# Kernel optimization log

Measured on AMD Instinct MI355X. Metric: run time of the kernel, lower is better.

Reference implementation:

```python
import jax, jax.numpy as jnp
import numpy as np

L_SEQ = 512
BATCH = 16
D_IN = 41
H = 800
ALPHABET_SIZE = 20
# standard RGN backbone geometry (picometers / radians): N-CA, CA-C, C-N
BOND_LENGTHS = np.array([145.801, 152.326, 132.868], dtype=np.float32)
BOND_ANGLES = np.array([2.124, 1.941, 2.028], dtype=np.float32)


def _lstm_dir(x, W_ih, W_hh, b_ih, b_hh, reverse):
    # x: [L, B, D]; PyTorch gate order i, f, g, o
    B = x.shape[1]
    Hh = W_hh.shape[1]
    xs = x[::-1] if reverse else x
    pre = jnp.einsum('lbd,gd->lbg', xs, W_ih) + b_ih + b_hh  # [L, B, 4H]

    def step(carry, p):
        h, c = carry
        g = p + h @ W_hh.T
        i, f, gg, o = jnp.split(g, 4, axis=-1)
        c = jax.nn.sigmoid(f) * c + jax.nn.sigmoid(i) * jnp.tanh(gg)
        h = jax.nn.sigmoid(o) * jnp.tanh(c)
        return (h, c), h

    h0 = jnp.zeros((B, Hh), x.dtype)
    _, hs = jax.lax.scan(step, (h0, h0), pre)
    return hs[::-1] if reverse else hs


def _normalize(v):
    return v / (jnp.linalg.norm(v, axis=-1, keepdims=True) + 1e-8)


def calculate_dihedrals(p, alphabet):
    # p: [L, B, A] mixture weights; alphabet: [A, 3] learned dihedral angles
    return jnp.arctan2(p @ jnp.sin(alphabet), p @ jnp.cos(alphabet))  # [L, B, 3]


def calculate_coordinates(dihedrals):
    # dihedrals: [L, B, 3] -> backbone coords [3L, B, 3] via sequential NeRF extension
    L, B, _ = dihedrals.shape
    phi = jnp.transpose(dihedrals, (0, 2, 1)).reshape(L * 3, B)  # [3L, B]
    r = jnp.asarray(np.tile(BOND_LENGTHS, L))       # [3L]
    theta = jnp.asarray(np.tile(BOND_ANGLES, L))    # [3L]
    # initial reference frame (three seed atoms)
    a = jnp.zeros((B, 3), dihedrals.dtype)
    b = jnp.tile(jnp.array([BOND_LENGTHS[0], 0.0, 0.0], dihedrals.dtype), (B, 1))
    ang = np.pi - BOND_ANGLES[0]
    c = b + jnp.array([BOND_LENGTHS[1] * np.cos(ang), BOND_LENGTHS[1] * np.sin(ang), 0.0], dihedrals.dtype)

    def step(carry, inp):
        p_a, p_b, p_c = carry
        r_i, th_i, ph_i = inp  # scalar, scalar, [B]
        st, ct = jnp.sin(th_i), jnp.cos(th_i)
        d2 = jnp.stack([-r_i * ct * jnp.ones_like(ph_i),
                        r_i * st * jnp.cos(ph_i),
                        r_i * st * jnp.sin(ph_i)], axis=-1)      # [B, 3]
        bc = _normalize(p_c - p_b)
        n = _normalize(jnp.cross(p_b - p_a, bc))
        m = jnp.stack([bc, jnp.cross(n, bc), n], axis=-1)        # [B, 3, 3]
        d = jnp.einsum('bij,bj->bi', m, d2) + p_c
        return (p_b, p_c, d), d

    _, coords = jax.lax.scan(step, (a, b, c), (r, theta, phi))
    return coords  # [3L, B, 3]


def setup_inputs() -> dict:
    keys = iter(jax.random.split(jax.random.key(0), 24))
    s = 1.0 / np.sqrt(H)

    def u(shape):
        return jax.random.uniform(next(keys), shape, jnp.float32, -s, s)

    inp = {'x': jax.random.normal(next(keys), (BATCH, L_SEQ, D_IN), jnp.float32)}
    for layer, din in ((0, D_IN), (1, 2 * H)):
        for d in ('f', 'b'):
            inp['W_ih_l%d%s' % (layer, d)] = u((4 * H, din))
            inp['W_hh_l%d%s' % (layer, d)] = u((4 * H, H))
            inp['b_ih_l%d%s' % (layer, d)] = u((4 * H,))
            inp['b_hh_l%d%s' % (layer, d)] = u((4 * H,))
    inp['W_lin'] = u((ALPHABET_SIZE, 2 * H))
    inp['b_lin'] = u((ALPHABET_SIZE,))
    inp['alphabet'] = jax.random.uniform(next(keys), (ALPHABET_SIZE, 3), jnp.float32, -np.pi, np.pi)
    return inp


def reference(x, W_ih_l0f, W_hh_l0f, b_ih_l0f, b_hh_l0f,
              W_ih_l0b, W_hh_l0b, b_ih_l0b, b_hh_l0b,
              W_ih_l1f, W_hh_l1f, b_ih_l1f, b_hh_l1f,
              W_ih_l1b, W_hh_l1b, b_ih_l1b, b_hh_l1b,
              W_lin, b_lin, alphabet):
    xs = jnp.transpose(x, (1, 0, 2))  # [L, B, D] (seq-major like nn.LSTM default)
    hf = _lstm_dir(xs, W_ih_l0f, W_hh_l0f, b_ih_l0f, b_hh_l0f, False)
    hb = _lstm_dir(xs, W_ih_l0b, W_hh_l0b, b_ih_l0b, b_hh_l0b, True)
    h1 = jnp.concatenate([hf, hb], axis=-1)  # [L, B, 2H] (dropout=0.4 off in eval)
    hf2 = _lstm_dir(h1, W_ih_l1f, W_hh_l1f, b_ih_l1f, b_hh_l1f, False)
    hb2 = _lstm_dir(h1, W_ih_l1b, W_hh_l1b, b_ih_l1b, b_hh_l1b, True)
    out = jnp.concatenate([hf2, hb2], axis=-1)  # [L, B, 2H]
    logits = out @ W_lin.T + b_lin              # [L, B, ALPHABET_SIZE]
    p = jax.nn.softmax(logits, axis=1)          # faithful: nn.Softmax(dim=1)
    dih = calculate_dihedrals(p, alphabet)      # [L, B, 3]
    return calculate_coordinates(dih)           # [3L, B, 3]
```

## Files before the change

### kernel.cpp

```cpp
#include <hip/hip_runtime.h>
#include <math.h>

#define L_SEQ 512
#define BATCH 16
#define D_IN  41
#define HD    800
#define G4    3200
#define A2H   1600
#define NA    20
#define NWG   50

#define OFF_A   ((size_t)0)
#define OFF_B   (OFF_A + (size_t)L_SEQ * BATCH * G4)
#define OFF_H   (OFF_B + (size_t)L_SEQ * BATCH * G4)
#define OFF_DIH (OFF_H + (size_t)L_SEQ * BATCH * A2H)
#define OFF_BAR (OFF_DIH + (size_t)L_SEQ * BATCH * 3)
#define FLG_STRIDE 32
#define NREP 8
#define DIR_STRIDE (NREP * NWG * FLG_STRIDE)
#define LAUNCH_STRIDE (2 * DIR_STRIDE)

static __device__ __forceinline__ float sigf(float x) {
    return 1.0f / (1.0f + __expf(-x));
}

static __device__ __forceinline__ void fbar3(int* flg, int wg, int v) {
    __syncthreads();
    if (threadIdx.x < NREP)
        __hip_atomic_store(flg + ((int)threadIdx.x * NWG + wg) * FLG_STRIDE, v,
                           __ATOMIC_RELAXED, __HIP_MEMORY_SCOPE_AGENT);
    if (threadIdx.x < 64) {
        int* base = flg + ((wg & (NREP - 1)) * NWG) * FLG_STRIDE;
        for (;;) {
            int v1 = (threadIdx.x < NWG)
                         ? __hip_atomic_load(base + (int)threadIdx.x * FLG_STRIDE,
                                             __ATOMIC_RELAXED, __HIP_MEMORY_SCOPE_AGENT)
                         : v;
            if (__all(v1 >= v)) break;
        }
    }
    __syncthreads();
}

__global__ void init_bar_kernel(int* bar) {
    for (int i = blockIdx.x * 256 + threadIdx.x; i < 2 * LAUNCH_STRIDE;
         i += gridDim.x * 256)
        bar[i] = 0;
}

__global__ void pre0_kernel(const float* __restrict__ x,
                            const float* __restrict__ Wf, const float* __restrict__ bif,
                            const float* __restrict__ bhf,
                            const float* __restrict__ Wb, const float* __restrict__ bib,
                            const float* __restrict__ bhb,
                            float* __restrict__ outF, float* __restrict__ outB) {
    const int tid = threadIdx.x;
    const int wg = blockIdx.x * 4 + (tid >> 6);
    if (wg >= NWG) return;
    const int rl = tid & 63;
    const int gate = rl >> 4, j = rl & 15;
    const int g = gate * 800 + wg * 16 + j;
    const int m = blockIdx.y;
    const int dir = blockIdx.z;
    const int b = m & 15, t = m >> 4;
    const float* W  = dir ? Wb  : Wf;
    const float* bi = dir ? bib : bif;
    const float* bh = dir ? bhb : bhf;
    float acc = bi[g] + bh[g];
    const float* xr = x + ((size_t)b * L_SEQ + t) * D_IN;
    const float* wr = W + (size_t)g * D_IN;
    #pragma unroll
    for (int d = 0; d < D_IN; ++d) acc = fmaf(xr[d], wr[d], acc);
    (dir ? outB : outF)[((size_t)wg * (L_SEQ * BATCH) + m) * 64 + rl] = acc;
}

__launch_bounds__(512, 1)
__global__ void recur_kernel(const float* __restrict__ preF, const float* __restrict__ preB,
                             const float* __restrict__ WhhF, const float* __restrict__ WhhB,
                             float* __restrict__ hout, int* __restrict__ bar) {
    __shared__ float uni[17920];
    __shared__ float gates[1024];
    const int tid = threadIdx.x;
    const int dir = blockIdx.x & 1;
    const int wg  = blockIdx.x >> 1;
    const int j0  = wg * 16;
    const float* pre = dir ? preB : preF;
    const float* Whh = dir ? WhhB : WhhF;
    int* flg = bar + dir * DIR_STRIDE;

    const int q = tid >> 5, c = tid & 31;
    float w[4][25];
    #pragma unroll
    for (int gi = 0; gi < 4; ++gi) {
        const float* wr = Whh + (size_t)(gi * HD + j0 + q) * HD + c;
        #pragma unroll
        for (int kk = 0; kk < 25; ++kk) w[gi][kk] = wr[kk * 32];
    }
    float cstate = 0.0f;

    const int b2 = tid >> 5, r2w2 = tid & 31;
    const int q2 = r2w2 >> 1, u2 = r2w2 & 1;

    const float* pre_wg = pre + (size_t)wg * (L_SEQ * BATCH) * 64;

    int ofs[7], lds[7];
    #pragma unroll
    for (int i = 0; i < 6; ++i) {
        int g = tid * 4 + i * 2048;
        int b = g / 800;
        int k = g - 800 * b;
        ofs[i] = 4 * (b * A2H + k);
        lds[i] = k * 17 + b;
    }
    {
        int g = 12288 + tid;
        int b = g / 800;
        int k = g - 800 * b;
        ofs[6] = 4 * (b * A2H + k);
        lds[6] = k * 17 + b;
    }

    for (int it = 0; it < L_SEQ; ++it) {
        const int t = dir ? (L_SEQ - 1 - it) : it;

        if (it == 0) {
            for (int i = tid; i < 13600; i += 512) uni[i] = 0.0f;
        } else {
            const int tprev = dir ? (L_SEQ - it) : (it - 1);
            const float* hsrc = hout + ((size_t)tprev * BATCH) * A2H + dir * HD;
            float4 rr[6];
            float r1f;
            asm volatile(
                "global_load_dwordx4 %0, %7, %14 sc0 sc1\n\t"
                "global_load_dwordx4 %1, %8, %14 sc0 sc1\n\t"
                "global_load_dwordx4 %2, %9, %14 sc0 sc1\n\t"
                "global_load_dwordx4 %3, %10, %14 sc0 sc1\n\t"
                "global_load_dwordx4 %4, %11, %14 sc0 sc1\n\t"
                "global_load_dwordx4 %5, %12, %14 sc0 sc1\n\t"
                "global_load_dword %6, %13, %14 sc0 sc1\n\t"
                "s_waitcnt vmcnt(0)"
                : "=&v"(rr[0]), "=&v"(rr[1]), "=&v"(rr[2]), "=&v"(rr[3]),
                  "=&v"(rr[4]), "=&v"(rr[5]), "=&v"(r1f)
                : "v"(ofs[0]), "v"(ofs[1]), "v"(ofs[2]), "v"(ofs[3]),
                  "v"(ofs[4]), "v"(ofs[5]), "v"(ofs[6]), "s"(hsrc)
                : "memory");
            #pragma unroll
            for (int i = 0; i < 6; ++i) {
                uni[lds[i]]      = rr[i].x;
                uni[lds[i] + 17] = rr[i].y;
                uni[lds[i] + 34] = rr[i].z;
                uni[lds[i] + 51] = rr[i].w;
            }
            uni[lds[6]] = r1f;
        }

        float pv[2];
        #pragma unroll
        for (int half = 0; half < 2; ++half) {
            const int rl_o = (2 * half + u2) * 16 + q2;
            pv[half] = pre_wg[((size_t)t * BATCH + b2) * 64 + rl_o];
        }
        __syncthreads();

        float acc[4][16];
        #pragma unroll
        for (int gi = 0; gi < 4; ++gi)
            #pragma unroll
            for (int b = 0; b < 16; ++b) acc[gi][b] = 0.0f;
        #pragma unroll
        for (int kk = 0; kk < 25; ++kk) {
            const int kb = (c + kk * 32) * 17;
            float hreg[16];
            #pragma unroll
            for (int b = 0; b < 16; ++b) hreg[b] = uni[kb + b];
            #pragma unroll
            for (int gi = 0; gi < 4; ++gi)
                #pragma unroll
                for (int b = 0; b < 16; ++b)
                    acc[gi][b] = fmaf(w[gi][kk], hreg[b], acc[gi][b]);
        }
        __syncthreads();

        #pragma unroll
        for (int half = 0; half < 2; ++half) {
            #pragma unroll
            for (int u = 0; u < 2; ++u) {
                const int r2w = q * 2 + u;
                #pragma unroll
                for (int b = 0; b < 16; ++b)
                    uni[(b * 32 + r2w) * 35 + c] = acc[2 * half + u][b];
            }
            __syncthreads();
            {
                float s = pv[half];
                const int base = (b2 * 32 + r2w2) * 35;
                #pragma unroll
                for (int cc = 0; cc < 32; ++cc) s += uni[base + cc];
                const int rl_o = (2 * half + u2) * 16 + q2;
                gates[rl_o * 16 + b2] = s;
            }
            __syncthreads();
        }

        if (tid < 256) {
            const int jj = tid >> 4, b = tid & 15;
            float ig = gates[(0 * 16 + jj) * 16 + b];
            float fg = gates[(1 * 16 + jj) * 16 + b];
            float gg = gates[(2 * 16 + jj) * 16 + b];
            float og = gates[(3 * 16 + jj) * 16 + b];
            float cn = sigf(fg) * cstate + sigf(ig) * tanhf(gg);
            cstate = cn;
            float hn = sigf(og) * tanhf(cn);
            __hip_atomic_store(&hout[((size_t)t * BATCH + b) * A2H + dir * HD + j0 + jj],
                               hn, __ATOMIC_RELAXED, __HIP_MEMORY_SCOPE_AGENT);
        }
        if (it < L_SEQ - 1) fbar3(flg, wg, it + 1);
    }
}

static __device__ __forceinline__ int permn(int np) {
    return ((np & 63) >> 4) * 800 + (np >> 6) * 16 + (np & 15);
}

__launch_bounds__(256)
__global__ void gemm_pre1_kernel(const float* __restrict__ Ah,
                                 const float* __restrict__ WF, const float* __restrict__ biF,
                                 const float* __restrict__ bhF,
                                 const float* __restrict__ WB, const float* __restrict__ biB,
                                 const float* __restrict__ bhB,
                                 float* __restrict__ CF, float* __restrict__ CB) {
    __shared__ float As[16][132];
    __shared__ float Bs[16][132];
    const int dir = blockIdx.z;
    const float* Bw = dir ? WB : WF;
    const float* bi = dir ? biB : biF;
    const float* bh = dir ? bhB : bhF;
    float* C = dir ? CB : CF;
    const int n0 = blockIdx.x * 128;
    const int m0 = blockIdx.y * 128;
    const int tid = threadIdx.x;
    const int mt = tid >> 4, nt = tid & 15;
    const int r = tid >> 2, kq = tid & 3;
    const size_t nr0 = (size_t)permn(n0 + r) * A2H;
    const size_t nr1 = (size_t)permn(n0 + r + 64) * A2H;

    float acc[8][8];
    #pragma unroll
    for (int i = 0; i < 8; ++i)
        #pragma unroll
        for (int j = 0; j < 8; ++j) acc[i][j] = 0.0f;

    for (int k0 = 0; k0 < A2H; k0 += 16) {
        float4 a0 = *(const float4*)(Ah + (size_t)(m0 + r) * A2H + k0 + kq * 4);
        float4 a1 = *(const float4*)(Ah + (size_t)(m0 + r + 64) * A2H + k0 + kq * 4);
        float4 b0 = *(const float4*)(Bw + nr0 + k0 + kq * 4);
        float4 b1 = *(const float4*)(Bw + nr1 + k0 + kq * 4);
        __syncthreads();
        As[kq * 4 + 0][r] = a0.x;  As[kq * 4 + 1][r] = a0.y;
        As[kq * 4 + 2][r] = a0.z;  As[kq * 4 + 3][r] = a0.w;
        As[kq * 4 + 0][r + 64] = a1.x;  As[kq * 4 + 1][r + 64] = a1.y;
        As[kq * 4 + 2][r + 64] = a1.z;  As[kq * 4 + 3][r + 64] = a1.w;
        Bs[kq * 4 + 0][r] = b0.x;  Bs[kq * 4 + 1][r] = b0.y;
        Bs[kq * 4 + 2][r] = b0.z;  Bs[kq * 4 + 3][r] = b0.w;
        Bs[kq * 4 + 0][r + 64] = b1.x;  Bs[kq * 4 + 1][r + 64] = b1.y;
        Bs[kq * 4 + 2][r + 64] = b1.z;  Bs[kq * 4 + 3][r + 64] = b1.w;
        __syncthreads();
        #pragma unroll
        for (int kk = 0; kk < 16; ++kk) {
            float av[8], bv[8];
            #pragma unroll
            for (int j = 0; j < 8; ++j) av[j] = As[kk][mt * 8 + j];
            #pragma unroll
            for (int j = 0; j < 8; ++j) bv[j] = Bs[kk][nt * 8 + j];
            #pragma unroll
            for (int i = 0; i < 8; ++i)
                #pragma unroll
                for (int j = 0; j < 8; ++j)
                    acc[i][j] = fmaf(av[i], bv[j], acc[i][j]);
        }
    }
    float bias[8];
    #pragma unroll
    for (int j = 0; j < 8; ++j) {
        int n = permn(n0 + nt * 8 + j);
        bias[j] = bi[n] + bh[n];
    }
    const int npb = n0 + nt * 8;
    const int seg = npb >> 6;
    const int lo  = npb & 63;
    #pragma unroll
    for (int i = 0; i < 8; ++i) {
        float* dst = C + ((size_t)seg * (L_SEQ * BATCH) + (m0 + mt * 8 + i)) * 64 + lo;
        #pragma unroll
        for (int j = 0; j < 8; ++j) dst[j] = acc[i][j] + bias[j];
    }
}

__global__ void head_kernel(const float* __restrict__ out2,
                            const float* __restrict__ Wlin,
                            const float* __restrict__ blin,
                            const float* __restrict__ alphabet,
                            float* __restrict__ dih) {
    __shared__ float lg[16][21];
    __shared__ float sal[20][3], cal[20][3];
    const int t = blockIdx.x;
    const int tid = threadIdx.x;
    if (tid < 60) {
        int a = tid / 3, d = tid - 3 * (tid / 3);
        float v = alphabet[a * 3 + d];
        sal[a][d] = sinf(v);
        cal[a][d] = cosf(v);
    }
    const int b = tid / 20, a = tid - 20 * (tid / 20);
    const float* orow = out2 + ((size_t)t * BATCH + b) * A2H;
    const float* wrow = Wlin + (size_t)a * A2H;
    float s = blin[a];
    for (int k = 0; k < A2H; k += 4) {
        float4 ov = *(const float4*)(orow + k);
        float4 wv = *(const float4*)(wrow + k);
        s = fmaf(ov.x, wv.x, s);
        s = fmaf(ov.y, wv.y, s);
        s = fmaf(ov.z, wv.z, s);
        s = fmaf(ov.w, wv.w, s);
    }
    lg[b][a] = s;
    __syncthreads();
    if (tid < NA) {
        float mx = -1e30f;
        #pragma unroll
        for (int bb = 0; bb < BATCH; ++bb) mx = fmaxf(mx, lg[bb][tid]);
        float sum = 0.0f;
        #pragma unroll
        for (int bb = 0; bb < BATCH; ++bb) {
            float e = expf(lg[bb][tid] - mx);
            lg[bb][tid] = e;
            sum += e;
        }
        float inv = 1.0f / sum;
        #pragma unroll
        for (int bb = 0; bb < BATCH; ++bb) lg[bb][tid] *= inv;
    }
    __syncthreads();
    if (tid < 48) {
        int bb = tid / 3, dd = tid - 3 * (tid / 3);
        float ss = 0.0f, cc = 0.0f;
        #pragma unroll
        for (int aa = 0; aa < NA; ++aa) {
            float p = lg[bb][aa];
            ss = fmaf(p, sal[aa][dd], ss);
            cc = fmaf(p, cal[aa][dd], cc);
        }
        dih[((size_t)t * BATCH + bb) * 3 + dd] = atan2f(ss, cc);
    }
}

__global__ void nerf_kernel(const float* __restrict__ dih, float* __restrict__ out) {
    const int b = threadIdx.x;
    if (b >= BATCH) return;
    const float BL0 = 145.801f, BL1 = 152.326f, BL2 = 132.868f;
    const float BA0 = 2.124f,   BA1 = 1.941f,   BA2 = 2.028f;
    const float rr[3] = {BL0, BL1, BL2};
    const float st3[3] = {sinf(BA0), sinf(BA1), sinf(BA2)};
    const float ct3[3] = {cosf(BA0), cosf(BA1), cosf(BA2)};
    float ax = 0.f, ay = 0.f, az = 0.f;
    float bx = BL0, by = 0.f, bz = 0.f;
    float ang = 3.14159265358979323846f - BA0;
    float cx = bx + BL1 * cosf(ang), cy = BL1 * sinf(ang), cz = 0.f;
    for (int l = 0; l < L_SEQ; ++l) {
        #pragma unroll
        for (int d = 0; d < 3; ++d) {
            const int s = l * 3 + d;
            const float r = rr[d], st = st3[d], ct = ct3[d];
            float ph = dih[((size_t)l * BATCH + b) * 3 + d];
            float sp, cp;
            __sincosf(ph, &sp, &cp);
            float d2x = -r * ct, d2y = r * st * cp, d2z = r * st * sp;
            float bcx = cx - bx, bcy = cy - by, bcz = cz - bz;
            float inv = 1.0f / (sqrtf(bcx * bcx + bcy * bcy + bcz * bcz) + 1e-8f);
            bcx *= inv; bcy *= inv; bcz *= inv;
            float abx = bx - ax, aby = by - ay, abz = bz - az;
            float nx = aby * bcz - abz * bcy;
            float ny = abz * bcx - abx * bcz;
            float nz = abx * bcy - aby * bcx;
            inv = 1.0f / (sqrtf(nx * nx + ny * ny + nz * nz) + 1e-8f);
            nx *= inv; ny *= inv; nz *= inv;
            float m1x = ny * bcz - nz * bcy;
            float m1y = nz * bcx - nx * bcz;
            float m1z = nx * bcy - ny * bcx;
            float dx = bcx * d2x + m1x * d2y + nx * d2z + cx;
            float dy = bcy * d2x + m1y * d2y + ny * d2z + cy;
            float dz = bcz * d2x + m1z * d2y + nz * d2z + cz;
            size_t o = ((size_t)s * BATCH + b) * 3;
            out[o + 0] = dx; out[o + 1] = dy; out[o + 2] = dz;
            ax = bx; ay = by; az = bz;
            bx = cx; by = cy; bz = cz;
            cx = dx; cy = dy; cz = dz;
        }
    }
}

extern "C" void kernel_launch(void* const* d_in, const int* in_sizes, int n_in,
                              void* d_out, int out_size, void* d_ws, size_t ws_size,
                              hipStream_t stream) {
    (void)in_sizes; (void)n_in; (void)out_size; (void)ws_size;
    const float* x        = (const float*)d_in[0];
    const float* W_ih_l0f = (const float*)d_in[1];
    const float* W_hh_l0f = (const float*)d_in[2];
    const float* b_ih_l0f = (const float*)d_in[3];
    const float* b_hh_l0f = (const float*)d_in[4];
    const float* W_ih_l0b = (const float*)d_in[5];
    const float* W_hh_l0b = (const float*)d_in[6];
    const float* b_ih_l0b = (const float*)d_in[7];
    const float* b_hh_l0b = (const float*)d_in[8];
    const float* W_ih_l1f = (const float*)d_in[9];
    const float* W_hh_l1f = (const float*)d_in[10];
    const float* b_ih_l1f = (const float*)d_in[11];
    const float* b_hh_l1f = (const float*)d_in[12];
    const float* W_ih_l1b = (const float*)d_in[13];
    const float* W_hh_l1b = (const float*)d_in[14];
    const float* b_ih_l1b = (const float*)d_in[15];
    const float* b_hh_l1b = (const float*)d_in[16];
    const float* W_lin    = (const float*)d_in[17];
    const float* b_lin    = (const float*)d_in[18];
    const float* alphabet = (const float*)d_in[19];

    float* ws  = (float*)d_ws;
    float* bufA = ws + OFF_A;
    float* bufB = ws + OFF_B;
    float* h12  = ws + OFF_H;
    float* dih  = ws + OFF_DIH;
    int*   bar  = (int*)(ws + OFF_BAR);

    hipLaunchKernelGGL(init_bar_kernel, dim3(32), dim3(256), 0, stream, bar);

    hipLaunchKernelGGL(pre0_kernel, dim3(13, L_SEQ * BATCH, 2), dim3(256), 0, stream,
                       x, W_ih_l0f, b_ih_l0f, b_hh_l0f,
                       W_ih_l0b, b_ih_l0b, b_hh_l0b, bufA, bufB);

    {
        const float* a0 = bufA; const float* a1 = bufB;
        const float* a2 = W_hh_l0f; const float* a3 = W_hh_l0b;
        float* a4 = h12; int* a5 = bar;
        void* args[] = {&a0, &a1, &a2, &a3, &a4, &a5};
        hipError_t e = hipLaunchCooperativeKernel((const void*)recur_kernel, dim3(100),
                                                  dim3(512), args, 0, stream);
        (void)e;
    }

    hipLaunchKernelGGL(gemm_pre1_kernel, dim3(G4 / 128, (L_SEQ * BATCH) / 128, 2),
                       dim3(256), 0, stream,
                       h12, W_ih_l1f, b_ih_l1f, b_hh_l1f,
                       W_ih_l1b, b_ih_l1b, b_hh_l1b, bufA, bufB);

    {
        const float* a0 = bufA; const float* a1 = bufB;
        const float* a2 = W_hh_l1f; const float* a3 = W_hh_l1b;
        float* a4 = h12; int* a5 = bar + LAUNCH_STRIDE;
        void* args[] = {&a0, &a1, &a2, &a3, &a4, &a5};
        hipError_t e = hipLaunchCooperativeKernel((const void*)recur_kernel, dim3(100),
                                                  dim3(512), args, 0, stream);
        (void)e;
    }

    hipLaunchKernelGGL(head_kernel, dim3(L_SEQ), dim3(320), 0, stream,
                       h12, W_lin, b_lin, alphabet, dih);

    hipLaunchKernelGGL(nerf_kernel, dim3(1), dim3(64), 0, stream,
                       dih, (float*)d_out);
}
```

Measured before the change: 15.66 ms.

## Restructure recurrent kernel k-split for float4 LDS reads and single-pass reduction

Remaps threads in the persistent LSTM recurrence so each lane owns a contiguous 25-element k-slice, with h stored in LDS at stride 20 so four float4 loads fetch all 16 batch values. The cross-lane partial-sum reduction now goes through one shared buffer in a single pass instead of two halves with extra barriers, and the gate nonlinearity reads sums straight from registers. This cuts LDS instruction count and the number of barriers per timestep, at the cost of doubling the LDS footprint and possible bank conflicts in the new layout.

```diff
diff --git a/kernel.cpp b/kernel.cpp
--- a/kernel.cpp
+++ b/kernel.cpp
@@ -78,8 +78,7 @@
 __global__ void recur_kernel(const float* __restrict__ preF, const float* __restrict__ preB,
                              const float* __restrict__ WhhF, const float* __restrict__ WhhB,
                              float* __restrict__ hout, int* __restrict__ bar) {
-    __shared__ float uni[17920];
-    __shared__ float gates[1024];
+    __shared__ float uni[35840];
     const int tid = threadIdx.x;
     const int dir = blockIdx.x & 1;
     const int wg  = blockIdx.x >> 1;
@@ -88,18 +87,22 @@
     const float* Whh = dir ? WhhB : WhhF;
     int* flg = bar + dir * DIR_STRIDE;
 
-    const int q = tid >> 5, c = tid & 31;
+    const int wv = tid >> 6;
+    const int lane = tid & 63;
+    const int q = lane >> 2;
+    const int c = lane & 3;
+    const int k0 = wv * 100 + c * 25;
+    const int col2 = (4 * wv + c + 4 * q) & 31;
+
     float w[4][25];
     #pragma unroll
     for (int gi = 0; gi < 4; ++gi) {
-        const float* wr = Whh + (size_t)(gi * HD + j0 + q) * HD + c;
-        #pragma unroll
-        for (int kk = 0; kk < 25; ++kk) w[gi][kk] = wr[kk * 32];
+        const float* wr = Whh + (size_t)(gi * HD + j0 + q) * HD + k0;
+        #pragma unroll
+        for (int kk = 0; kk < 25; ++kk) w[gi][kk] = wr[kk];
     }
     float cstate = 0.0f;
-
-    const int b2 = tid >> 5, r2w2 = tid & 31;
-    const int q2 = r2w2 >> 1, u2 = r2w2 & 1;
+    const int jj2 = (tid >> 4) & 15, b2 = tid & 15;
 
     const float* pre_wg = pre + (size_t)wg * (L_SEQ * BATCH) * 64;
 
@@ -110,21 +113,21 @@
         int b = g / 800;
         int k = g - 800 * b;
         ofs[i] = 4 * (b * A2H + k);
-        lds[i] = k * 17 + b;
+        lds[i] = k * 20 + b;
     }
     {
         int g = 12288 + tid;
         int b = g / 800;
         int k = g - 800 * b;
         ofs[6] = 4 * (b * A2H + k);
-        lds[6] = k * 17 + b;
+        lds[6] = k * 20 + b;
     }
 
     for (int it = 0; it < L_SEQ; ++it) {
         const int t = dir ? (L_SEQ - 1 - it) : it;
 
         if (it == 0) {
-            for (int i = tid; i < 13600; i += 512) uni[i] = 0.0f;
+            for (int i = tid; i < 16000; i += 512) uni[i] = 0.0f;
         } else {
             const int tprev = dir ? (L_SEQ - it) : (it - 1);
             const float* hsrc = hout + ((size_t)tprev * BATCH) * A2H + dir * HD;
@@ -147,18 +150,18 @@
             #pragma unroll
             for (int i = 0; i < 6; ++i) {
                 uni[lds[i]]      = rr[i].x;
-                uni[lds[i] + 17] = rr[i].y;
-                uni[lds[i] + 34] = rr[i].z;
-                uni[lds[i] + 51] = rr[i].w;
+                uni[lds[i] + 20] = rr[i].y;
+                uni[lds[i] + 40] = rr[i].z;
+                uni[lds[i] + 60] = rr[i].w;
             }
             uni[lds[6]] = r1f;
         }
 
-        float pv[2];
-        #pragma unroll
-        for (int half = 0; half < 2; ++half) {
-            const int rl_o = (2 * half + u2) * 16 + q2;
-            pv[half] = pre_wg[((size_t)t * BATCH + b2) * 64 + rl_o];
+        float pv[4];
+        if (tid < 256) {
+            #pragma unroll
+            for (int gi = 0; gi < 4; ++gi)
+                pv[gi] = pre_wg[((size_t)t * BATCH + b2) * 64 + gi * 16 + jj2];
         }
         __syncthreads();
 
@@ -169,10 +172,13 @@
             for (int b = 0; b < 16; ++b) acc[gi][b] = 0.0f;
         #pragma unroll
         for (int kk = 0; kk < 25; ++kk) {
-            const int kb = (c + kk * 32) * 17;
-            float hreg[16];
-            #pragma unroll
-            for (int b = 0; b < 16; ++b) hreg[b] = uni[kb + b];
+            const float* hp = &uni[(k0 + kk) * 20];
+            float4 h0 = *(const float4*)(hp);
+            float4 h1 = *(const float4*)(hp + 4);
+            float4 h2 = *(const float4*)(hp + 8);
+            float4 h3 = *(const float4*)(hp + 12);
+            float hreg[16] = {h0.x, h0.y, h0.z, h0.w, h1.x, h1.y, h1.z, h1.w,
+                              h2.x, h2.y, h2.z, h2.w, h3.x, h3.y, h3.z, h3.w};
             #pragma unroll
             for (int gi = 0; gi < 4; ++gi)
                 #pragma unroll
@@ -182,36 +188,26 @@
         __syncthreads();
 
         #pragma unroll
-        for (int half = 0; half < 2; ++half) {
-            #pragma unroll
-            for (int u = 0; u < 2; ++u) {
-                const int r2w = q * 2 + u;
+        for (int gi = 0; gi < 4; ++gi)
+            #pragma unroll
+            for (int b = 0; b < 16; ++b)
+                uni[((gi * 16 + q) * 16 + b) * 35 + col2] = acc[gi][b];
+        __syncthreads();
+
+        if (tid < 256) {
+            float s[4];
+            #pragma unroll
+            for (int gi = 0; gi < 4; ++gi) {
+                const int base = ((gi * 16 + jj2) * 16 + b2) * 35;
+                float acc2 = pv[gi];
                 #pragma unroll
-                for (int b = 0; b < 16; ++b)
-                    uni[(b * 32 + r2w) * 35 + c] = acc[2 * half + u][b];
+                for (int col = 0; col < 32; ++col) acc2 += uni[base + col];
+                s[gi] = acc2;
             }
-            __syncthreads();
-            {
-                float s = pv[half];
-                const int base = (b2 * 32 + r2w2) * 35;
-                #pragma unroll
-                for (int cc = 0; cc < 32; ++cc) s += uni[base + cc];
-                const int rl_o = (2 * half + u2) * 16 + q2;
-                gates[rl_o * 16 + b2] = s;
-            }
-            __syncthreads();
-        }
-
-        if (tid < 256) {
-            const int jj = tid >> 4, b = tid & 15;
-            float ig = gates[(0 * 16 + jj) * 16 + b];
-            float fg = gates[(1 * 16 + jj) * 16 + b];
-            float gg = gates[(2 * 16 + jj) * 16 + b];
-            float og = gates[(3 * 16 + jj) * 16 + b];
-            float cn = sigf(fg) * cstate + sigf(ig) * tanhf(gg);
+            float cn = sigf(s[1]) * cstate + sigf(s[0]) * tanhf(s[2]);
             cstate = cn;
-            float hn = sigf(og) * tanhf(cn);
-            __hip_atomic_store(&hout[((size_t)t * BATCH + b) * A2H + dir * HD + j0 + jj],
+            float hn = sigf(s[3]) * tanhf(cn);
+            __hip_atomic_store(&hout[((size_t)t * BATCH + b2) * A2H + dir * HD + j0 + jj2],
                                hn, __ATOMIC_RELAXED, __HIP_MEMORY_SCOPE_AGENT);
         }
         if (it < L_SEQ - 1) fbar3(flg, wg, it + 1);
```

After: 14.17 ms. 1.11x faster.
